# Kernel tuning notes

Hardware: AMD Instinct MI355X
Metric: run time of the kernel (lower is better)

## Reference

```python
import jax, jax.numpy as jnp
import numpy as np
import math

N_EMBD = 1024
BLOCK_SIZE = 2048
B = 4

def setup_inputs() -> dict:
    key = jax.random.key(0)
    ks = jax.random.split(key, 9)
    s = 0.02
    return {
        "q": jax.random.normal(ks[0], (B, BLOCK_SIZE, N_EMBD), jnp.float32),
        "k": jax.random.normal(ks[1], (B, BLOCK_SIZE, N_EMBD), jnp.float32),
        "v": jax.random.normal(ks[2], (B, BLOCK_SIZE, N_EMBD), jnp.float32),
        "wq_w": jax.random.normal(ks[3], (N_EMBD, N_EMBD), jnp.float32) * s,
        "wq_b": jax.random.normal(ks[4], (N_EMBD,), jnp.float32) * s,
        "wk_w": jax.random.normal(ks[5], (N_EMBD, N_EMBD), jnp.float32) * s,
        "wk_b": jax.random.normal(ks[6], (N_EMBD,), jnp.float32) * s,
        "wv_w": jax.random.normal(ks[7], (N_EMBD, N_EMBD), jnp.float32) * s,
        "wv_b": jax.random.normal(ks[8], (N_EMBD,), jnp.float32) * s,
        "causal": 1,
    }

def reference(q, k, v, wq_w, wq_b, wk_w, wk_b, wv_w, wv_b, causal):
    # torch Linear: y = x @ W.T + b
    qp = jnp.einsum('bte,oe->bto', q, wq_w) + wq_b
    kp = jnp.einsum('bte,oe->bto', k, wk_w) + wk_b
    vp = jnp.einsum('bte,oe->bto', v, wv_w) + wv_b
    scale = 1.0 / math.sqrt(N_EMBD)
    weights = jnp.einsum('bqe,bke->bqk', qp, kp) * scale  # [B,T1,T2]
    if causal:
        T1, T2 = qp.shape[1], kp.shape[1]
        mask = jnp.tril(jnp.ones((T1, T2), dtype=bool))
        weights = jnp.where(mask, weights, -jnp.inf)
    attn = jax.nn.softmax(weights, axis=-1)
    return jnp.einsum('bqk,bke->bqe', attn, vp)
```

## Files before the change

kernel.cpp:

```cpp
#include <hip/hip_runtime.h>
#include <hip/hip_bf16.h>
#include <cstdint>
#include <math.h>

#define T 2048
#define NE 1024
#define NB 4

typedef __attribute__((ext_vector_type(8))) short short8;
typedef __attribute__((ext_vector_type(4))) short shortx4;
typedef __attribute__((ext_vector_type(4))) float floatx4;

__device__ __forceinline__ unsigned short f2bf(float f) {
    unsigned u = __float_as_uint(f);
    u += 0x7FFF + ((u >> 16) & 1);
    return (unsigned short)(u >> 16);
}

__device__ __forceinline__ shortx4 cvt4(floatx4 f) {
    __hip_bfloat162 a = __float22bfloat162_rn(float2{f[0], f[1]});
    __hip_bfloat162 b = __float22bfloat162_rn(float2{f[2], f[3]});
    union { shortx4 s; unsigned u[2]; } r;
    r.u[0] = *(unsigned*)&a; r.u[1] = *(unsigned*)&b;
    return r.s;
}

__device__ __forceinline__ void gl2lds(const void* g, void* l) {
    __builtin_amdgcn_global_load_lds(
        (const __attribute__((address_space(1))) void*)g,
        (__attribute__((address_space(3))) void*)l, 16, 0, 0);
}

template<int NWROW, int BIAS_MODE, bool OUT_F32, bool CKLIM, bool DUAL, int MODE>
__global__ __launch_bounds__(NWROW * 128, 4) void gemm_bf16(
    const unsigned short* __restrict__ A0, const unsigned short* __restrict__ A1,
    const unsigned short* __restrict__ B0, const unsigned short* __restrict__ B1,
    const float* __restrict__ bias0, const float* __restrict__ bias1,
    void* __restrict__ C0, void* __restrict__ C1,
    int K, int lda, int ldb, int ldc,
    size_t sA, size_t sB, size_t sC, float scale, int ntnShift)
{
    constexpr int NTHR = NWROW * 128;
    int tm, tn;
    const int bz = blockIdx.z;
    if (MODE == 2) {
        const int i = blockIdx.x;
        int lin = (i & 7) * 17 + (i >> 3);
        tm = (int)((sqrtf(8.f * (float)lin + 1.f) - 1.f) * 0.5f);
        while ((tm + 1) * (tm + 2) / 2 <= lin) ++tm;
        while (tm * (tm + 1) / 2 > lin) --tm;
        tn = lin - tm * (tm + 1) / 2;
    } else if (MODE == 1) {
        const int bid = blockIdx.x;
        const int lin = (bid & 7) * (gridDim.x >> 3) + (bid >> 3);
        tm = lin >> ntnShift; tn = lin & ((1 << ntnShift) - 1);
    } else if (MODE == 3) {
        const int xcd = blockIdx.x & 7, j = blockIdx.x >> 3;
        tm = (j & 1) ? xcd : (15 - xcd);
        tn = j >> 1;
    } else {
        tn = blockIdx.x; tm = blockIdx.y;
    }

    __shared__ __align__(16) char As[NWROW * 64 * 128];
    __shared__ __align__(16) char Bs[128 * 128];

    const int tid = threadIdx.x, lane = tid & 63, wave = tid >> 6;
    const int wm = wave % NWROW, wn = wave / NWROW;
    const int quad = lane >> 4, l15 = lane & 15;
    const int p = l15 & 7;
    const int r8 = lane >> 3, c8 = lane & 7;

    const char* Ab = (const char*)((DUAL && bz) ? A1 : A0) + (size_t)bz * sA * 2;
    const char* Bb = (const char*)((DUAL && bz) ? B1 : B0) + (size_t)bz * sB * 2;
    const float* bias = (DUAL && bz) ? bias1 : bias0;

    int Keff = K;
    if (CKLIM) { int kl = (tm + 1) * 128; Keff = kl < K ? kl : K; }

    const size_t ldab = (size_t)lda * 2, ldbb = (size_t)ldb * 2;
    const char* gA = Ab + (size_t)(tm * (NWROW * 64) + wave * 8 + r8) * ldab + (size_t)((c8 ^ r8) * 16);
    const char* gB = Bb + (size_t)(tn * 128 + wave * 8 + r8) * ldbb + (size_t)((c8 ^ r8) * 16);
    char* lA = As + wave * 1024;
    char* lB = Bs + wave * 1024;
    constexpr int BCALLS = 8 / NWROW;

    floatx4 acc[4][4] = {};

    for (int k0 = 0; k0 < Keff; k0 += 64) {
        const size_t kb = (size_t)k0 * 2;
        #pragma unroll
        for (int c = 0; c < 4; ++c)
            gl2lds(gA + (size_t)(c * NWROW * 16) * ldab + kb, lA + c * NTHR * 16);
        #pragma unroll
        for (int c = 0; c < BCALLS; ++c)
            gl2lds(gB + (size_t)(c * NWROW * 16) * ldbb + kb, lB + c * NTHR * 16);
        __syncthreads();

        #pragma unroll
        for (int kk = 0; kk < 2; kk++) {
            short8 af[4], bfr[4];
            #pragma unroll
            for (int i = 0; i < 4; i++)
                af[i] = *(const short8*)(As + (wm * 64 + i * 16 + l15) * 128 + (((kk * 4 + quad) ^ p) << 4));
            #pragma unroll
            for (int j = 0; j < 4; j++)
                bfr[j] = *(const short8*)(Bs + (wn * 64 + j * 16 + l15) * 128 + (((kk * 4 + quad) ^ p) << 4));
            #pragma unroll
            for (int i = 0; i < 4; i++)
                #pragma unroll
                for (int j = 0; j < 4; j++)
                    acc[i][j] = __builtin_amdgcn_mfma_f32_16x16x32_bf16(af[i], bfr[j], acc[i][j], 0, 0, 0);
        }
        __syncthreads();
    }

    char* Cb = (char*)((DUAL && bz) ? C1 : C0) + (size_t)bz * sC * (OUT_F32 ? 4 : 2);
    #pragma unroll
    for (int i = 0; i < 4; i++) {
        #pragma unroll
        for (int j = 0; j < 4; j++) {
            const int n = tn * 128 + wn * 64 + j * 16 + l15;
            #pragma unroll
            for (int r = 0; r < 4; r++) {
                const int m = tm * (NWROW * 64) + wm * 64 + i * 16 + quad * 4 + r;
                float val = acc[i][j][r] * scale;
                if (BIAS_MODE == 1) val += bias[n];
                if (BIAS_MODE == 2) val += bias[m];
                if (OUT_F32) ((float*)Cb)[(size_t)m * ldc + n] = val;
                else         ((unsigned short*)Cb)[(size_t)m * ldc + n] = f2bf(val);
            }
        }
    }
}

__global__ __launch_bounds__(256) void cvt_all(
    const float* __restrict__ q, const float* __restrict__ k, const float* __restrict__ v,
    const float* __restrict__ wq, const float* __restrict__ wk, const float* __restrict__ wv,
    unsigned short* __restrict__ qb, unsigned short* __restrict__ kb, unsigned short* __restrict__ vb,
    unsigned short* __restrict__ wqb, unsigned short* __restrict__ wkb, unsigned short* __restrict__ wvb)
{
    const int IN4 = NB * T * NE / 4;
    const int W4  = NE * NE / 4;
    int i = blockIdx.x * 256 + threadIdx.x;
    const float* s; unsigned short* d; int j;
    if (i < 3 * IN4) {
        int sel = i >> 21; j = i & (IN4 - 1);
        s = sel == 0 ? q : sel == 1 ? k : v;
        d = sel == 0 ? qb : sel == 1 ? kb : vb;
    } else {
        int t2 = i - 3 * IN4; int sel = t2 >> 18; j = t2 & (W4 - 1);
        s = sel == 0 ? wq : sel == 1 ? wk : wv;
        d = sel == 0 ? wqb : sel == 1 ? wkb : wvb;
    }
    floatx4 f = ((const floatx4*)s)[j];
    ((shortx4*)d)[j] = cvt4(f);
}

__global__ __launch_bounds__(256) void softmax_causal(unsigned short* __restrict__ S)
{
    const int row = blockIdx.x;
    const int b = row >> 11, r = row & 2047;
    unsigned short* p = S + ((size_t)b * T + (size_t)r) * T;
    const int nv = r + 1;
    const int lim = ((r >> 7) + 1) * 128;
    const int tid = threadIdx.x, lane = tid & 63, wave = tid >> 6;
    const int c0 = tid * 8;
    const bool act = c0 < lim;

    short8 raw = {};
    if (act) raw = ((const short8*)p)[tid];
    float x[8];
    float mx = -3.0e38f;
    #pragma unroll
    for (int j = 0; j < 8; j++) {
        float vv = -3.0e38f;
        if (c0 + j < nv) vv = __uint_as_float((unsigned)(unsigned short)raw[j] << 16);
        x[j] = vv;
        mx = fmaxf(mx, vv);
    }
    #pragma unroll
    for (int off = 32; off > 0; off >>= 1)
        mx = fmaxf(mx, __shfl_xor(mx, off));
    __shared__ float smax[4], ssum[4];
    if (lane == 0) smax[wave] = mx;
    __syncthreads();
    mx = fmaxf(fmaxf(smax[0], smax[1]), fmaxf(smax[2], smax[3]));

    float s = 0.f;
    #pragma unroll
    for (int j = 0; j < 8; j++) {
        float e = 0.f;
        if (c0 + j < nv) e = __expf(x[j] - mx);
        x[j] = e;
        s += e;
    }
    #pragma unroll
    for (int off = 32; off > 0; off >>= 1)
        s += __shfl_xor(s, off);
    if (lane == 0) ssum[wave] = s;
    __syncthreads();
    const float inv = 1.f / (ssum[0] + ssum[1] + ssum[2] + ssum[3]);

    if (act) {
        short8 o;
        #pragma unroll
        for (int j = 0; j < 8; j++)
            o[j] = (short)f2bf(x[j] * inv);
        ((short8*)p)[tid] = o;
    }
}

extern "C" void kernel_launch(void* const* d_in, const int* in_sizes, int n_in,
                              void* d_out, int out_size, void* d_ws, size_t ws_size,
                              hipStream_t stream)
{
    const float* q    = (const float*)d_in[0];
    const float* k    = (const float*)d_in[1];
    const float* v    = (const float*)d_in[2];
    const float* wq_w = (const float*)d_in[3];
    const float* wq_b = (const float*)d_in[4];
    const float* wk_w = (const float*)d_in[5];
    const float* wk_b = (const float*)d_in[6];
    const float* wv_w = (const float*)d_in[7];
    const float* wv_b = (const float*)d_in[8];

    const size_t INEL = (size_t)NB * T * NE;

    unsigned short* qp = (unsigned short*)d_out;
    unsigned short* kp = qp + INEL;

    unsigned short* vpT = (unsigned short*)d_ws;
    unsigned short* S   = vpT + (size_t)NB * NE * T;
    unsigned short* qb  = S;
    unsigned short* kb  = qb + INEL;
    unsigned short* vb  = kb + INEL;
    unsigned short* wqb = vb + INEL;
    unsigned short* wkb = wqb + (size_t)NE * NE;
    unsigned short* wvb = wkb + (size_t)NE * NE;

    dim3 blk(256);

    const int NCVT = (3 * (int)(INEL / 4) + 3 * NE * NE / 4 + 255) / 256;
    cvt_all<<<dim3(NCVT), blk, 0, stream>>>(q, k, v, wq_w, wk_w, wv_w, qb, kb, vb, wqb, wkb, wvb);

    gemm_bf16<4, 1, false, false, true, 1><<<dim3(256, 1, 2), dim3(512), 0, stream>>>(
        qb, kb, wqb, wkb, wq_b, wk_b, qp, kp, NE, NE, NE, NE, 0, 0, 0, 1.0f, 3);

    gemm_bf16<4, 2, false, false, false, 1><<<dim3(64, 1, NB), dim3(512), 0, stream>>>(
        wvb, nullptr, vb, nullptr, wv_b, nullptr, vpT, nullptr,
        NE, NE, NE, T, 0, (size_t)T * NE, (size_t)NE * T, 1.0f, 4);

    gemm_bf16<2, 0, false, false, false, 2><<<dim3(136, 1, NB), blk, 0, stream>>>(
        qp, nullptr, kp, nullptr, nullptr, nullptr, S, nullptr,
        NE, NE, NE, T, (size_t)T * NE, (size_t)T * NE, (size_t)T * T, 0.03125f, 0);

    softmax_causal<<<dim3(NB * T), blk, 0, stream>>>(S);

    gemm_bf16<2, 0, true, true, false, 3><<<dim3(128, 1, NB), blk, 0, stream>>>(
        S, nullptr, vpT, nullptr, nullptr, nullptr, d_out, nullptr,
        T, T, T, NE, (size_t)T * T, (size_t)NE * T, (size_t)T * NE, 1.0f, 0);
}
```

Before: 295.8 us.

## Fuse fp32-to-bf16 conversion of activations into projection GEMM tile loads

Removes the separate conversion pass over q, k and v. The projection GEMMs now read fp32 activations directly from global memory, convert them to bf16 in registers, and store them into LDS, keeping the swizzled layout. This avoids writing and rereading a bf16 copy of the three large inputs. The cost is that those GEMM operand loads become synchronous register loads instead of async global-to-LDS copies, and each tile fetches twice as many bytes.

```diff
diff --git a/kernel.cpp b/kernel.cpp
--- a/kernel.cpp
+++ b/kernel.cpp
@@ -25,13 +25,25 @@
     return r.s;
 }
 
+__device__ __forceinline__ short8 cvt8(floatx4 f0, floatx4 f1) {
+    __hip_bfloat162 a = __float22bfloat162_rn(float2{f0[0], f0[1]});
+    __hip_bfloat162 b = __float22bfloat162_rn(float2{f0[2], f0[3]});
+    __hip_bfloat162 c = __float22bfloat162_rn(float2{f1[0], f1[1]});
+    __hip_bfloat162 d = __float22bfloat162_rn(float2{f1[2], f1[3]});
+    union { short8 s; unsigned u[4]; } r;
+    r.u[0] = *(unsigned*)&a; r.u[1] = *(unsigned*)&b;
+    r.u[2] = *(unsigned*)&c; r.u[3] = *(unsigned*)&d;
+    return r.s;
+}
+
 __device__ __forceinline__ void gl2lds(const void* g, void* l) {
     __builtin_amdgcn_global_load_lds(
         (const __attribute__((address_space(1))) void*)g,
         (__attribute__((address_space(3))) void*)l, 16, 0, 0);
 }
 
-template<int NWROW, int BIAS_MODE, bool OUT_F32, bool CKLIM, bool DUAL, int MODE>
+template<int NWROW, int BIAS_MODE, bool OUT_F32, bool CKLIM, bool DUAL, int MODE,
+         bool AF32, bool BF32>
 __global__ __launch_bounds__(NWROW * 128, 4) void gemm_bf16(
     const unsigned short* __restrict__ A0, const unsigned short* __restrict__ A1,
     const unsigned short* __restrict__ B0, const unsigned short* __restrict__ B1,
@@ -41,6 +53,7 @@
     size_t sA, size_t sB, size_t sC, float scale, int ntnShift)
 {
     constexpr int NTHR = NWROW * 128;
+    constexpr int ABY = AF32 ? 4 : 2, BBY = BF32 ? 4 : 2;
     int tm, tn;
     const int bz = blockIdx.z;
     if (MODE == 2) {
@@ -71,16 +84,16 @@
     const int p = l15 & 7;
     const int r8 = lane >> 3, c8 = lane & 7;
 
-    const char* Ab = (const char*)((DUAL && bz) ? A1 : A0) + (size_t)bz * sA * 2;
-    const char* Bb = (const char*)((DUAL && bz) ? B1 : B0) + (size_t)bz * sB * 2;
+    const char* Ab = (const char*)((DUAL && bz) ? A1 : A0) + (size_t)bz * sA * ABY;
+    const char* Bb = (const char*)((DUAL && bz) ? B1 : B0) + (size_t)bz * sB * BBY;
     const float* bias = (DUAL && bz) ? bias1 : bias0;
 
     int Keff = K;
     if (CKLIM) { int kl = (tm + 1) * 128; Keff = kl < K ? kl : K; }
 
-    const size_t ldab = (size_t)lda * 2, ldbb = (size_t)ldb * 2;
-    const char* gA = Ab + (size_t)(tm * (NWROW * 64) + wave * 8 + r8) * ldab + (size_t)((c8 ^ r8) * 16);
-    const char* gB = Bb + (size_t)(tn * 128 + wave * 8 + r8) * ldbb + (size_t)((c8 ^ r8) * 16);
+    const size_t ldab = (size_t)lda * ABY, ldbb = (size_t)ldb * BBY;
+    const char* gA = Ab + (size_t)(tm * (NWROW * 64) + wave * 8 + r8) * ldab + (size_t)((c8 ^ r8) * (AF32 ? 32 : 16));
+    const char* gB = Bb + (size_t)(tn * 128 + wave * 8 + r8) * ldbb + (size_t)((c8 ^ r8) * (BF32 ? 32 : 16));
     char* lA = As + wave * 1024;
     char* lB = Bs + wave * 1024;
     constexpr int BCALLS = 8 / NWROW;
@@ -88,13 +101,42 @@
     floatx4 acc[4][4] = {};
 
     for (int k0 = 0; k0 < Keff; k0 += 64) {
-        const size_t kb = (size_t)k0 * 2;
-        #pragma unroll
-        for (int c = 0; c < 4; ++c)
-            gl2lds(gA + (size_t)(c * NWROW * 16) * ldab + kb, lA + c * NTHR * 16);
-        #pragma unroll
-        for (int c = 0; c < BCALLS; ++c)
-            gl2lds(gB + (size_t)(c * NWROW * 16) * ldbb + kb, lB + c * NTHR * 16);
+        const size_t kbA = (size_t)k0 * ABY;
+        const size_t kbB = (size_t)k0 * BBY;
+        if constexpr (AF32) {
+            #pragma unroll
+            for (int c = 0; c < 4; c += 2) {
+                const char* s0 = gA + (size_t)(c * NWROW * 16) * ldab + kbA;
+                const char* s1 = gA + (size_t)((c + 1) * NWROW * 16) * ldab + kbA;
+                floatx4 f0a = *(const floatx4*)(s0);
+                floatx4 f0b = *(const floatx4*)(s0 + 16);
+                floatx4 f1a = *(const floatx4*)(s1);
+                floatx4 f1b = *(const floatx4*)(s1 + 16);
+                *(short8*)(lA + c * NTHR * 16 + lane * 16)       = cvt8(f0a, f0b);
+                *(short8*)(lA + (c + 1) * NTHR * 16 + lane * 16) = cvt8(f1a, f1b);
+            }
+        } else {
+            #pragma unroll
+            for (int c = 0; c < 4; ++c)
+                gl2lds(gA + (size_t)(c * NWROW * 16) * ldab + kbA, lA + c * NTHR * 16);
+        }
+        if constexpr (BF32) {
+            #pragma unroll
+            for (int c = 0; c < BCALLS; c += 2) {
+                const char* s0 = gB + (size_t)(c * NWROW * 16) * ldbb + kbB;
+                const char* s1 = gB + (size_t)((c + 1) * NWROW * 16) * ldbb + kbB;
+                floatx4 f0a = *(const floatx4*)(s0);
+                floatx4 f0b = *(const floatx4*)(s0 + 16);
+                floatx4 f1a = *(const floatx4*)(s1);
+                floatx4 f1b = *(const floatx4*)(s1 + 16);
+                *(short8*)(lB + c * NTHR * 16 + lane * 16)       = cvt8(f0a, f0b);
+                *(short8*)(lB + (c + 1) * NTHR * 16 + lane * 16) = cvt8(f1a, f1b);
+            }
+        } else {
+            #pragma unroll
+            for (int c = 0; c < BCALLS; ++c)
+                gl2lds(gB + (size_t)(c * NWROW * 16) * ldbb + kbB, lB + c * NTHR * 16);
+        }
         __syncthreads();
 
         #pragma unroll
@@ -134,25 +176,15 @@
     }
 }
 
-__global__ __launch_bounds__(256) void cvt_all(
-    const float* __restrict__ q, const float* __restrict__ k, const float* __restrict__ v,
+__global__ __launch_bounds__(256) void cvt_w(
     const float* __restrict__ wq, const float* __restrict__ wk, const float* __restrict__ wv,
-    unsigned short* __restrict__ qb, unsigned short* __restrict__ kb, unsigned short* __restrict__ vb,
     unsigned short* __restrict__ wqb, unsigned short* __restrict__ wkb, unsigned short* __restrict__ wvb)
 {
-    const int IN4 = NB * T * NE / 4;
-    const int W4  = NE * NE / 4;
+    const int W4 = NE * NE / 4;
     int i = blockIdx.x * 256 + threadIdx.x;
-    const float* s; unsigned short* d; int j;
-    if (i < 3 * IN4) {
-        int sel = i >> 21; j = i & (IN4 - 1);
-        s = sel == 0 ? q : sel == 1 ? k : v;
-        d = sel == 0 ? qb : sel == 1 ? kb : vb;
-    } else {
-        int t2 = i - 3 * IN4; int sel = t2 >> 18; j = t2 & (W4 - 1);
-        s = sel == 0 ? wq : sel == 1 ? wk : wv;
-        d = sel == 0 ? wqb : sel == 1 ? wkb : wvb;
-    }
+    int sel = i >> 18, j = i & (W4 - 1);
+    const float* s = sel == 0 ? wq : sel == 1 ? wk : wv;
+    unsigned short* d = sel == 0 ? wqb : sel == 1 ? wkb : wvb;
     floatx4 f = ((const floatx4*)s)[j];
     ((shortx4*)d)[j] = cvt4(f);
 }
@@ -232,32 +264,30 @@
 
     unsigned short* vpT = (unsigned short*)d_ws;
     unsigned short* S   = vpT + (size_t)NB * NE * T;
-    unsigned short* qb  = S;
-    unsigned short* kb  = qb + INEL;
-    unsigned short* vb  = kb + INEL;
-    unsigned short* wqb = vb + INEL;
+    unsigned short* wqb = S;
     unsigned short* wkb = wqb + (size_t)NE * NE;
     unsigned short* wvb = wkb + (size_t)NE * NE;
 
     dim3 blk(256);
 
-    const int NCVT = (3 * (int)(INEL / 4) + 3 * NE * NE / 4 + 255) / 256;
-    cvt_all<<<dim3(NCVT), blk, 0, stream>>>(q, k, v, wq_w, wk_w, wv_w, qb, kb, vb, wqb, wkb, wvb);
-
-    gemm_bf16<4, 1, false, false, true, 1><<<dim3(256, 1, 2), dim3(512), 0, stream>>>(
-        qb, kb, wqb, wkb, wq_b, wk_b, qp, kp, NE, NE, NE, NE, 0, 0, 0, 1.0f, 3);
-
-    gemm_bf16<4, 2, false, false, false, 1><<<dim3(64, 1, NB), dim3(512), 0, stream>>>(
-        wvb, nullptr, vb, nullptr, wv_b, nullptr, vpT, nullptr,
+    const int NCVT = 3 * (NE * NE / 4) / 256;
+    cvt_w<<<dim3(NCVT), blk, 0, stream>>>(wq_w, wk_w, wv_w, wqb, wkb, wvb);
+
+    gemm_bf16<4, 1, false, false, true, 1, true, false><<<dim3(256, 1, 2), dim3(512), 0, stream>>>(
+        (const unsigned short*)q, (const unsigned short*)k, wqb, wkb, wq_b, wk_b,
+        qp, kp, NE, NE, NE, NE, 0, 0, 0, 1.0f, 3);
+
+    gemm_bf16<4, 2, false, false, false, 1, false, true><<<dim3(64, 1, NB), dim3(512), 0, stream>>>(
+        wvb, nullptr, (const unsigned short*)v, nullptr, wv_b, nullptr, vpT, nullptr,
         NE, NE, NE, T, 0, (size_t)T * NE, (size_t)NE * T, 1.0f, 4);
 
-    gemm_bf16<2, 0, false, false, false, 2><<<dim3(136, 1, NB), blk, 0, stream>>>(
+    gemm_bf16<2, 0, false, false, false, 2, false, false><<<dim3(136, 1, NB), blk, 0, stream>>>(
         qp, nullptr, kp, nullptr, nullptr, nullptr, S, nullptr,
         NE, NE, NE, T, (size_t)T * NE, (size_t)T * NE, (size_t)T * T, 0.03125f, 0);
 
     softmax_causal<<<dim3(NB * T), blk, 0, stream>>>(S);
 
-    gemm_bf16<2, 0, true, true, false, 3><<<dim3(128, 1, NB), blk, 0, stream>>>(
+    gemm_bf16<2, 0, true, true, false, 3, false, false><<<dim3(128, 1, NB), blk, 0, stream>>>(
         S, nullptr, vpT, nullptr, nullptr, nullptr, d_out, nullptr,
         T, T, T, NE, (size_t)T * T, (size_t)NE * T, (size_t)T * NE, 1.0f, 0);
 }
```

Result: slower. 315.9 us (+6.8%).
